# Kernel optimization log

Hardware: AMD Instinct MI355X
Metric: run time of the kernel (lower is better)

Reference implementation:

```python
import math
import jax, jax.numpy as jnp
import numpy as np

B, T, D, H = 4, 2048, 256, 4
DK = D // H
P = 2 * T - 1  # relative position length


def setup_inputs() -> dict:
    key = jax.random.key(0)
    ks = jax.random.split(key, 16)
    s = 0.02
    inp = {
        "query": jax.random.normal(ks[0], (B, T, D), jnp.float32),
        "key": jax.random.normal(ks[1], (B, T, D), jnp.float32),
        "value": jax.random.normal(ks[2], (B, T, D), jnp.float32),
        "pos_emb": jax.random.normal(ks[3], (1, P, D), jnp.float32),
        "mask": jnp.ones((B, 1, T), jnp.int32),
        "Wq": jax.random.normal(ks[4], (D, D), jnp.float32) * s,
        "bq": jnp.zeros((D,), jnp.float32),
        "Wk": jax.random.normal(ks[5], (D, D), jnp.float32) * s,
        "bk": jnp.zeros((D,), jnp.float32),
        "Wv": jax.random.normal(ks[6], (D, D), jnp.float32) * s,
        "bv": jnp.zeros((D,), jnp.float32),
        "Wpos": jax.random.normal(ks[7], (D, D), jnp.float32) * s,
        "pos_bias_u": jax.random.normal(ks[8], (H, DK), jnp.float32) * s,
        "pos_bias_v": jax.random.normal(ks[9], (H, DK), jnp.float32) * s,
        "Wo": jax.random.normal(ks[10], (D, D), jnp.float32) * s,
        "bo": jnp.zeros((D,), jnp.float32),
    }
    return inp


def rel_shift(x):
    # x: (B, H, T, P) with P = 2T-1  ->  (B, H, T, T)
    b, h, t, p = x.shape
    x_pad = jnp.pad(x, ((0, 0), (0, 0), (0, 0), (1, 0)))  # (B,H,T,P+1)
    x_pad = x_pad.reshape(b, h, p + 1, t)
    x = x_pad[:, :, 1:].reshape(b, h, t, p)
    return x[..., : p // 2 + 1]


def reference(query, key, value, pos_emb, mask, Wq, bq, Wk, bk, Wv, bv,
              Wpos, pos_bias_u, pos_bias_v, Wo, bo):
    b = query.shape[0]
    q = (query @ Wq.T + bq).reshape(b, -1, H, DK)              # (B,T,H,DK)
    k = (key @ Wk.T + bk).reshape(b, -1, H, DK).transpose(0, 2, 1, 3)    # (B,H,T,DK)
    v = (value @ Wv.T + bv).reshape(b, -1, H, DK).transpose(0, 2, 1, 3)  # (B,H,T,DK)
    p = (pos_emb @ Wpos.T).reshape(pos_emb.shape[0], -1, H, DK).transpose(0, 2, 1, 3)  # (1,H,P,DK)

    q_u = (q + pos_bias_u).transpose(0, 2, 1, 3)  # (B,H,T,DK)
    q_v = (q + pos_bias_v).transpose(0, 2, 1, 3)

    matrix_ac = jnp.matmul(q_u, k.transpose(0, 1, 3, 2))  # (B,H,T,T)
    matrix_bd = jnp.matmul(q_v, p.transpose(0, 1, 3, 2))  # (B,H,T,P), batch broadcast
    matrix_bd = rel_shift(matrix_bd)                       # (B,H,T,T)

    scores = (matrix_ac + matrix_bd) / math.sqrt(DK)
    m = (mask[:, None] == 0)  # (B,1,1,T) bool
    scores = jnp.where(m, jnp.float32(-1e9), scores)
    attn = jax.nn.softmax(scores, axis=-1)
    attn = jnp.where(m, jnp.float32(0.0), attn)

    x = jnp.matmul(attn, v)                               # (B,H,T,DK)
    x = x.transpose(0, 2, 1, 3).reshape(b, -1, H * DK)    # (B,T,D)
    return x @ Wo.T + bo
```

## Files before the change

### kernel.cpp

```cpp
#include <hip/hip_runtime.h>
#include <hip/hip_bf16.h>
#include <string.h>

#define Bc 4
#define Tc 2048
#define Dc 256
#define Hc 4
#define DKc 64
#define Pc 4095

typedef short bf16x8 __attribute__((ext_vector_type(8)));
typedef float f32x4 __attribute__((ext_vector_type(4)));

__device__ __forceinline__ unsigned short f2bs(float x) {
    __bf16 b = (__bf16)x;
    return __builtin_bit_cast(unsigned short, b);
}
__device__ __forceinline__ float bs2f(unsigned short u) {
    unsigned int x = ((unsigned int)u) << 16;
    return __builtin_bit_cast(float, x);
}

__global__ __launch_bounds__(256) void wsplit_kernel(
    const float* __restrict__ W,
    unsigned short* __restrict__ Whi,
    unsigned short* __restrict__ Wlo)
{
    int i = blockIdx.x * 256 + threadIdx.x;
    if (i >= Dc * Dc) return;
    float w = W[i];
    unsigned short h = f2bs(w);
    Whi[i] = h;
    Wlo[i] = f2bs(w - bs2f(h));
}

__global__ __launch_bounds__(256) void gemm_mfma_proj(
    const float* __restrict__ A,
    const float* __restrict__ Wt,
    const float* __restrict__ bias,
    const float* __restrict__ addv,
    unsigned short* __restrict__ outp,
    int M, int Tdim)
{
    __shared__ unsigned short sa[64 * 72];
    __shared__ unsigned short sb[64 * 72];
    const int tid = threadIdx.x;
    const int wv = tid >> 6, lane = tid & 63;
    const int c = lane & 15, g = lane >> 4;
    const int m0 = blockIdx.x * 64, n0 = blockIdx.y * 64;
    const int tb = wv * 16;

    f32x4 acc[4];
    #pragma unroll
    for (int ct = 0; ct < 4; ct++) acc[ct] = (f32x4){0.f, 0.f, 0.f, 0.f};

    for (int k0 = 0; k0 < 256; k0 += 64) {
        if (k0) __syncthreads();
        #pragma unroll
        for (int r = 0; r < 2; r++) {
            int lin = tid + 256 * r;
            int row = lin >> 3, ch = lin & 7;
            int gm = m0 + row;
            float4 f0, f1;
            if (gm < M) {
                f0 = *(const float4*)(A + (size_t)gm * 256 + k0 + ch * 8);
                f1 = *(const float4*)(A + (size_t)gm * 256 + k0 + ch * 8 + 4);
            } else {
                f0 = make_float4(0.f, 0.f, 0.f, 0.f); f1 = f0;
            }
            unsigned short pa[8] = {f2bs(f0.x), f2bs(f0.y), f2bs(f0.z), f2bs(f0.w),
                                    f2bs(f1.x), f2bs(f1.y), f2bs(f1.z), f2bs(f1.w)};
            *(uint4*)&sa[row * 72 + ch * 8] = *(const uint4*)pa;

            float4 w0 = *(const float4*)(Wt + (size_t)(n0 + row) * 256 + k0 + ch * 8);
            float4 w1 = *(const float4*)(Wt + (size_t)(n0 + row) * 256 + k0 + ch * 8 + 4);
            unsigned short pb[8] = {f2bs(w0.x), f2bs(w0.y), f2bs(w0.z), f2bs(w0.w),
                                    f2bs(w1.x), f2bs(w1.y), f2bs(w1.z), f2bs(w1.w)};
            *(uint4*)&sb[row * 72 + ch * 8] = *(const uint4*)pb;
        }
        __syncthreads();
        #pragma unroll
        for (int kk = 0; kk < 2; kk++) {
            bf16x8 af = *(const bf16x8*)&sa[(tb + c) * 72 + kk * 32 + g * 8];
            #pragma unroll
            for (int ct = 0; ct < 4; ct++) {
                bf16x8 bf = *(const bf16x8*)&sb[(ct * 16 + c) * 72 + kk * 32 + g * 8];
                acc[ct] = __builtin_amdgcn_mfma_f32_16x16x32_bf16(af, bf, acc[ct], 0, 0, 0);
            }
        }
    }

    __syncthreads();
    #pragma unroll
    for (int ct = 0; ct < 4; ct++) {
        int n = n0 + ct * 16 + c;
        float badd = (bias ? bias[n] : 0.f) + (addv ? addv[n] : 0.f);
        #pragma unroll
        for (int r = 0; r < 4; r++)
            sa[(tb + g * 4 + r) * 72 + ct * 16 + c] = f2bs(acc[ct][r] + badd);
    }
    __syncthreads();
    const int hh = n0 >> 6;
    #pragma unroll
    for (int r = 0; r < 2; r++) {
        int lin = tid + 256 * r;
        int row = lin >> 3, ch = lin & 7;
        int gm = m0 + row;
        if (gm >= M) continue;
        int bb = gm / Tdim, t = gm - bb * Tdim;
        size_t oidx = ((size_t)(bb * Hc + hh) * Tdim + t) * DKc + ch * 8;
        *(uint4*)&outp[oidx] = *(const uint4*)&sa[row * 72 + ch * 8];
    }
}

__global__ __launch_bounds__(256) void gemm_out_split(
    const unsigned short* __restrict__ Ahi,
    const unsigned short* __restrict__ Alo,
    const unsigned short* __restrict__ Whi,
    const unsigned short* __restrict__ Wlo,
    const float* __restrict__ bias,
    float* __restrict__ outp, int M)
{
    __shared__ unsigned short sah[64 * 72];
    __shared__ unsigned short sal[64 * 72];
    __shared__ unsigned short sbh[64 * 72];
    __shared__ unsigned short sbl[64 * 72];
    __shared__ float sout[64 * 68];
    const int tid = threadIdx.x;
    const int wv = tid >> 6, lane = tid & 63;
    const int c = lane & 15, g = lane >> 4;
    const int m0 = blockIdx.x * 64, n0 = blockIdx.y * 64;
    const int tb = wv * 16;

    f32x4 acc[4];
    #pragma unroll
    for (int ct = 0; ct < 4; ct++) acc[ct] = (f32x4){0.f, 0.f, 0.f, 0.f};

    for (int k0 = 0; k0 < 256; k0 += 64) {
        if (k0) __syncthreads();
        #pragma unroll
        for (int r = 0; r < 2; r++) {
            int lin = tid + 256 * r;
            int row = lin >> 3, ch = lin & 7;
            size_t asrc = (size_t)(m0 + row) * 256 + k0 + ch * 8;
            size_t wsrc = (size_t)(n0 + row) * 256 + k0 + ch * 8;
            *(uint4*)&sah[row * 72 + ch * 8] = *(const uint4*)(Ahi + asrc);
            *(uint4*)&sal[row * 72 + ch * 8] = *(const uint4*)(Alo + asrc);
            *(uint4*)&sbh[row * 72 + ch * 8] = *(const uint4*)(Whi + wsrc);
            *(uint4*)&sbl[row * 72 + ch * 8] = *(const uint4*)(Wlo + wsrc);
        }
        __syncthreads();
        #pragma unroll
        for (int kk = 0; kk < 2; kk++) {
            bf16x8 ah = *(const bf16x8*)&sah[(tb + c) * 72 + kk * 32 + g * 8];
            bf16x8 al = *(const bf16x8*)&sal[(tb + c) * 72 + kk * 32 + g * 8];
            #pragma unroll
            for (int ct = 0; ct < 4; ct++) {
                bf16x8 bh = *(const bf16x8*)&sbh[(ct * 16 + c) * 72 + kk * 32 + g * 8];
                bf16x8 bl = *(const bf16x8*)&sbl[(ct * 16 + c) * 72 + kk * 32 + g * 8];
                acc[ct] = __builtin_amdgcn_mfma_f32_16x16x32_bf16(ah, bh, acc[ct], 0, 0, 0);
                acc[ct] = __builtin_amdgcn_mfma_f32_16x16x32_bf16(ah, bl, acc[ct], 0, 0, 0);
                acc[ct] = __builtin_amdgcn_mfma_f32_16x16x32_bf16(al, bh, acc[ct], 0, 0, 0);
            }
        }
    }

    __syncthreads();
    #pragma unroll
    for (int ct = 0; ct < 4; ct++) {
        float b = bias[n0 + ct * 16 + c];
        #pragma unroll
        for (int r = 0; r < 4; r++)
            sout[(tb + g * 4 + r) * 68 + ct * 16 + c] = acc[ct][r] + b;
    }
    __syncthreads();
    #pragma unroll
    for (int r = 0; r < 4; r++) {
        int lin = tid + 256 * r;
        int row = lin >> 4, c4 = lin & 15;
        float4 v = *(const float4*)&sout[row * 68 + c4 * 4];
        *(float4*)&outp[(size_t)(m0 + row) * 256 + n0 + c4 * 4] = v;
    }
}

__global__ __launch_bounds__(256) void dpw_kernel(
    const unsigned short* __restrict__ ph,
    const float* __restrict__ pbu,
    const float* __restrict__ pbv,
    float* __restrict__ dpw)
{
    int idx = blockIdx.x * 256 + threadIdx.x;
    if (idx >= Hc * Pc) return;
    int h = idx / Pc;
    const unsigned short* row = ph + (size_t)idx * DKc;
    const float* u = pbu + h * DKc;
    const float* v = pbv + h * DKc;
    float acc = 0.f;
    #pragma unroll
    for (int d = 0; d < DKc; d++)
        acc = fmaf(v[d] - u[d], bs2f(row[d]), acc);
    dpw[idx] = acc;
}

__global__ __launch_bounds__(256) void attn_mfma(
    const unsigned short* __restrict__ qu,
    const unsigned short* __restrict__ kh,
    const unsigned short* __restrict__ vh,
    const unsigned short* __restrict__ ph,
    const float* __restrict__ dpw_g,
    const int*   __restrict__ mask,
    unsigned short* __restrict__ xhi,
    unsigned short* __restrict__ xlo)
{
    __shared__ unsigned short sq[64 * 72];
    __shared__ unsigned short sk[64 * 72];
    __shared__ unsigned short svt[64 * 72];
    __shared__ unsigned short sp[64 * 72];
    __shared__ unsigned short spw[128 * 72];
    __shared__ float sbdw[4][16 * 84];
    __shared__ float sdpw[128];
    __shared__ float smask[64];

    const int tid = threadIdx.x;
    const int wv = tid >> 6;
    const int lane = tid & 63;
    const int c = lane & 15, g = lane >> 4;
    const int bh = blockIdx.x, b = bh >> 2, h = bh & 3;
    const int t0 = blockIdx.y * 64;
    const int tb = wv * 16;

    const unsigned short* qbase = qu + ((size_t)bh * Tc + t0) * DKc;
    const unsigned short* kbase = kh + (size_t)bh * Tc * DKc;
    const unsigned short* vbase = vh + (size_t)bh * Tc * DKc;
    const unsigned short* pbase = ph + (size_t)h * Pc * DKc;

    #pragma unroll
    for (int r = 0; r < 2; r++) {
        int lin = tid + 256 * r;
        int row = lin >> 3, ch = lin & 7;
        *(uint4*)&sq[row * 72 + ch * 8] =
            *(const uint4*)(qbase + (size_t)row * DKc + ch * 8);
    }

    f32x4 O[4];
    #pragma unroll
    for (int ct = 0; ct < 4; ct++) O[ct] = (f32x4){0.f, 0.f, 0.f, 0.f};
    float mrow[4], lrow[4];
    #pragma unroll
    for (int r = 0; r < 4; r++) { mrow[r] = -3.0e38f; lrow[r] = 0.f; }

    bf16x8 qf0, qf1;

    for (int kt = 0; kt < Tc / 64; kt++) {
        const int j0 = kt * 64;
        __syncthreads();

        #pragma unroll
        for (int r = 0; r < 2; r++) {
            int lin = tid + 256 * r;
            int row = lin >> 3, ch = lin & 7;
            *(uint4*)&sk[row * 72 + ch * 8] =
                *(const uint4*)(kbase + (size_t)(j0 + row) * DKc + ch * 8);
        }
        #pragma unroll
        for (int r = 0; r < 2; r++) {
            int lin = tid + 256 * r;
            int trow = lin >> 3, ch = lin & 7;
            uint4 raw = *(const uint4*)(vbase + (size_t)(j0 + trow) * DKc + ch * 8);
            unsigned short el[8];
            __builtin_memcpy(el, &raw, 16);
            #pragma unroll
            for (int e = 0; e < 8; e++) {
                int dk = ch * 8 + e;
                svt[dk * 72 + (trow ^ ((dk >> 3) << 3))] = el[e];
            }
        }
        const int relbase = j0 - t0 + (Tc - 64);
        #pragma unroll
        for (int r = 0; r < 4; r++) {
            int lin = tid + 256 * r;
            int row = lin >> 3, ch = lin & 7;
            int grow = relbase + row;
            if (grow > Pc - 1) grow = Pc - 1;
            *(uint4*)&spw[row * 72 + ch * 8] =
                *(const uint4*)(pbase + (size_t)grow * DKc + ch * 8);
        }
        if (tid < 128) {
            int idx = relbase + tid;
            sdpw[tid] = (idx <= Pc - 1) ? dpw_g[h * Pc + idx] : 0.f;
        }
        if (tid < 64) smask[tid] = (mask[b * Tc + j0 + tid] == 0) ? -1e9f : 0.f;
        __syncthreads();

        if (kt == 0) {
            qf0 = *(const bf16x8*)&sq[(tb + c) * 72 + g * 8];
            qf1 = *(const bf16x8*)&sq[(tb + c) * 72 + (4 + g) * 8];
        }

        f32x4 sac[4];
        #pragma unroll
        for (int ct = 0; ct < 4; ct++) {
            f32x4 acc = (f32x4){0.f, 0.f, 0.f, 0.f};
            bf16x8 kf0 = *(const bf16x8*)&sk[(ct * 16 + c) * 72 + g * 8];
            bf16x8 kf1 = *(const bf16x8*)&sk[(ct * 16 + c) * 72 + (4 + g) * 8];
            acc = __builtin_amdgcn_mfma_f32_16x16x32_bf16(qf0, kf0, acc, 0, 0, 0);
            acc = __builtin_amdgcn_mfma_f32_16x16x32_bf16(qf1, kf1, acc, 0, 0, 0);
            sac[ct] = acc;
        }

        #pragma unroll
        for (int wt = 0; wt < 5; wt++) {
            f32x4 acc = (f32x4){0.f, 0.f, 0.f, 0.f};
            int prow = (48 - tb) + wt * 16 + c;
            bf16x8 pf0 = *(const bf16x8*)&spw[prow * 72 + g * 8];
            bf16x8 pf1 = *(const bf16x8*)&spw[prow * 72 + (4 + g) * 8];
            acc = __builtin_amdgcn_mfma_f32_16x16x32_bf16(qf0, pf0, acc, 0, 0, 0);
            acc = __builtin_amdgcn_mfma_f32_16x16x32_bf16(qf1, pf1, acc, 0, 0, 0);
            float dpwv = sdpw[(48 - tb) + wt * 16 + c];
            #pragma unroll
            for (int r = 0; r < 4; r++)
                sbdw[wv][(g * 4 + r) * 84 + wt * 16 + c] = acc[r] + dpwv;
        }

        float sreg[4][4];
        #pragma unroll
        for (int ct = 0; ct < 4; ct++) {
            float madd = smask[ct * 16 + c];
            #pragma unroll
            for (int r = 0; r < 4; r++) {
                int tt = g * 4 + r;
                int x = ct * 16 + c - tt + 15;
                sreg[ct][r] = (sac[ct][r] + sbdw[wv][tt * 84 + x]) * 0.125f + madd;
            }
        }

        float tmax[4], tsum[4];
        #pragma unroll
        for (int r = 0; r < 4; r++)
            tmax[r] = fmaxf(fmaxf(sreg[0][r], sreg[1][r]), fmaxf(sreg[2][r], sreg[3][r]));
        #pragma unroll
        for (int off = 1; off < 16; off <<= 1)
            #pragma unroll
            for (int r = 0; r < 4; r++)
                tmax[r] = fmaxf(tmax[r], __shfl_xor(tmax[r], off));

        float mnew[4], scl[4];
        #pragma unroll
        for (int r = 0; r < 4; r++) {
            mnew[r] = fmaxf(mrow[r], tmax[r]);
            scl[r] = __expf(mrow[r] - mnew[r]);
        }
        float pr[4][4];
        #pragma unroll
        for (int r = 0; r < 4; r++) {
            #pragma unroll
            for (int ct = 0; ct < 4; ct++)
                pr[ct][r] = __expf(sreg[ct][r] - mnew[r]);
            tsum[r] = (pr[0][r] + pr[1][r]) + (pr[2][r] + pr[3][r]);
        }
        #pragma unroll
        for (int off = 1; off < 16; off <<= 1)
            #pragma unroll
            for (int r = 0; r < 4; r++)
                tsum[r] += __shfl_xor(tsum[r], off);
        #pragma unroll
        for (int r = 0; r < 4; r++) {
            lrow[r] = lrow[r] * scl[r] + tsum[r];
            mrow[r] = mnew[r];
        }
        #pragma unroll
        for (int ct = 0; ct < 4; ct++) {
            f32x4 o = O[ct];
            o[0] *= scl[0]; o[1] *= scl[1]; o[2] *= scl[2]; o[3] *= scl[3];
            O[ct] = o;
        }

        #pragma unroll
        for (int ct = 0; ct < 4; ct++)
            #pragma unroll
            for (int r = 0; r < 4; r++)
                sp[(tb + g * 4 + r) * 72 + ct * 16 + c] = f2bs(pr[ct][r]);

        #pragma unroll
        for (int js = 0; js < 2; js++) {
            bf16x8 pfrag = *(const bf16x8*)&sp[(tb + c) * 72 + (js * 4 + g) * 8];
            #pragma unroll
            for (int ct = 0; ct < 4; ct++) {
                int dk = ct * 16 + c;
                int tcol = (js * 32 + g * 8) ^ ((dk >> 3) << 3);
                bf16x8 vf = *(const bf16x8*)&svt[dk * 72 + tcol];
                O[ct] = __builtin_amdgcn_mfma_f32_16x16x32_bf16(pfrag, vf, O[ct], 0, 0, 0);
            }
        }
    }

    float invl[4];
    #pragma unroll
    for (int r = 0; r < 4; r++)
        invl[r] = (lrow[r] > 0.f) ? 1.f / lrow[r] : 0.f;
    #pragma unroll
    for (int ct = 0; ct < 4; ct++)
        #pragma unroll
        for (int r = 0; r < 4; r++) {
            size_t idx = ((size_t)(b * Tc + t0 + tb + g * 4 + r)) * Dc + h * DKc + ct * 16 + c;
            float v = O[ct][r] * invl[r];
            unsigned short hi = f2bs(v);
            xhi[idx] = hi;
            xlo[idx] = f2bs(v - bs2f(hi));
        }
}

extern "C" void kernel_launch(void* const* d_in, const int* in_sizes, int n_in,
                              void* d_out, int out_size, void* d_ws, size_t ws_size,
                              hipStream_t stream) {
    const float* query   = (const float*)d_in[0];
    const float* key_    = (const float*)d_in[1];
    const float* value   = (const float*)d_in[2];
    const float* pos_emb = (const float*)d_in[3];
    const int*   mask    = (const int*)d_in[4];
    const float* Wq  = (const float*)d_in[5];
    const float* bq  = (const float*)d_in[6];
    const float* Wk  = (const float*)d_in[7];
    const float* bk  = (const float*)d_in[8];
    const float* Wv  = (const float*)d_in[9];
    const float* bv  = (const float*)d_in[10];
    const float* Wpos = (const float*)d_in[11];
    const float* pbu = (const float*)d_in[12];
    const float* pbv = (const float*)d_in[13];
    const float* Wo  = (const float*)d_in[14];
    const float* bo  = (const float*)d_in[15];
    float* out = (float*)d_out;

    const size_t NQ = (size_t)Bc * Hc * Tc * DKc;
    unsigned short* qu_b = (unsigned short*)d_ws;
    unsigned short* kh_b = qu_b + NQ;
    unsigned short* vh_b = kh_b + NQ;
    unsigned short* ph_b = vh_b + NQ;
    unsigned short* xhi  = ph_b + 1048576;
    unsigned short* xlo  = xhi + NQ;
    unsigned short* wo_hi = xlo + NQ;
    unsigned short* wo_lo = wo_hi + 65536;
    float* dpw = (float*)(wo_lo + 65536);

    dim3 blk(256);
    wsplit_kernel<<<dim3(Dc * Dc / 256), blk, 0, stream>>>(Wo, wo_hi, wo_lo);
    gemm_mfma_proj<<<dim3(128, 4), blk, 0, stream>>>(query, Wq, bq, pbu, qu_b, Bc * Tc, Tc);
    gemm_mfma_proj<<<dim3(128, 4), blk, 0, stream>>>(key_,  Wk, bk, nullptr, kh_b, Bc * Tc, Tc);
    gemm_mfma_proj<<<dim3(128, 4), blk, 0, stream>>>(value, Wv, bv, nullptr, vh_b, Bc * Tc, Tc);
    gemm_mfma_proj<<<dim3(64, 4),  blk, 0, stream>>>(pos_emb, Wpos, nullptr, nullptr, ph_b, Pc, Pc);
    dpw_kernel<<<dim3((Hc * Pc + 255) / 256), blk, 0, stream>>>(ph_b, pbu, pbv, dpw);
    attn_mfma<<<dim3(Bc * Hc, Tc / 64), blk, 0, stream>>>(qu_b, kh_b, vh_b, ph_b, dpw, mask, xhi, xlo);
    gemm_out_split<<<dim3(128, 4), blk, 0, stream>>>(xhi, xlo, wo_hi, wo_lo, bo, out, Bc * Tc);
}
```

Measured before the change: 246.9 us.

## Merge launches, fold scale into Q, and register-prefetch K/V/P in attention

Merges the Q/K/V projections into one launch over blockIdx.z and fuses the dpw reduction into the positional projection. The Wo hi/lo split now happens inside the output GEMM, and the 1/sqrt(dk) scale is folded into Q and dpw. The attention loop now prefetches the next K, V and P tiles, plus dpw and mask, into registers while the current tile is computed, and keeps P in a 128-row ring buffer so each step loads 64 new rows instead of 128. The aim is fewer launches and less exposed global-load latency, at the cost of more register pressure and redundant Wo splitting in every output block.

```diff
diff --git a/kernel.cpp b/kernel.cpp
--- a/kernel.cpp
+++ b/kernel.cpp
@@ -21,29 +21,12 @@
     return __builtin_bit_cast(float, x);
 }
 
-__global__ __launch_bounds__(256) void wsplit_kernel(
-    const float* __restrict__ W,
-    unsigned short* __restrict__ Whi,
-    unsigned short* __restrict__ Wlo)
+__device__ __forceinline__ void gemm_body(
+    const float* __restrict__ A, const float* __restrict__ Wt,
+    const float* __restrict__ bias, const float* __restrict__ addv,
+    unsigned short* __restrict__ outp, int M, int Tdim, float scale,
+    unsigned short* sa, unsigned short* sb)
 {
-    int i = blockIdx.x * 256 + threadIdx.x;
-    if (i >= Dc * Dc) return;
-    float w = W[i];
-    unsigned short h = f2bs(w);
-    Whi[i] = h;
-    Wlo[i] = f2bs(w - bs2f(h));
-}
-
-__global__ __launch_bounds__(256) void gemm_mfma_proj(
-    const float* __restrict__ A,
-    const float* __restrict__ Wt,
-    const float* __restrict__ bias,
-    const float* __restrict__ addv,
-    unsigned short* __restrict__ outp,
-    int M, int Tdim)
-{
-    __shared__ unsigned short sa[64 * 72];
-    __shared__ unsigned short sb[64 * 72];
     const int tid = threadIdx.x;
     const int wv = tid >> 6, lane = tid & 63;
     const int c = lane & 15, g = lane >> 4;
@@ -97,7 +80,7 @@
         float badd = (bias ? bias[n] : 0.f) + (addv ? addv[n] : 0.f);
         #pragma unroll
         for (int r = 0; r < 4; r++)
-            sa[(tb + g * 4 + r) * 72 + ct * 16 + c] = f2bs(acc[ct][r] + badd);
+            sa[(tb + g * 4 + r) * 72 + ct * 16 + c] = f2bs((acc[ct][r] + badd) * scale);
     }
     __syncthreads();
     const int hh = n0 >> 6;
@@ -113,11 +96,51 @@
     }
 }
 
+__global__ __launch_bounds__(256) void gemm_qkv(
+    const float* __restrict__ q, const float* __restrict__ k, const float* __restrict__ v,
+    const float* __restrict__ Wq, const float* __restrict__ bq,
+    const float* __restrict__ Wk, const float* __restrict__ bk,
+    const float* __restrict__ Wv, const float* __restrict__ bv,
+    const float* __restrict__ pbu,
+    unsigned short* __restrict__ qo, unsigned short* __restrict__ ko,
+    unsigned short* __restrict__ vo)
+{
+    __shared__ unsigned short sa[64 * 72];
+    __shared__ unsigned short sb[64 * 72];
+    const float *A, *Wt, *bias, *addv; unsigned short* outp; float scale;
+    if (blockIdx.z == 0)      { A = q; Wt = Wq; bias = bq; addv = pbu;    outp = qo; scale = 0.125f; }
+    else if (blockIdx.z == 1) { A = k; Wt = Wk; bias = bk; addv = nullptr; outp = ko; scale = 1.f; }
+    else                      { A = v; Wt = Wv; bias = bv; addv = nullptr; outp = vo; scale = 1.f; }
+    gemm_body(A, Wt, bias, addv, outp, Bc * Tc, Tc, scale, sa, sb);
+}
+
+__global__ __launch_bounds__(256) void gemm_p(
+    const float* __restrict__ pos_emb, const float* __restrict__ Wpos,
+    const float* __restrict__ pbu, const float* __restrict__ pbv,
+    unsigned short* __restrict__ ph_b, float* __restrict__ dpw)
+{
+    __shared__ unsigned short sa[64 * 72];
+    __shared__ unsigned short sb[64 * 72];
+    gemm_body(pos_emb, Wpos, nullptr, nullptr, ph_b, Pc, Pc, 1.f, sa, sb);
+    const int tid = threadIdx.x;
+    const int m0 = blockIdx.x * 64, h = blockIdx.y;
+    if (tid < 64) {
+        int w = m0 + tid;
+        if (w < Pc) {
+            float acc = 0.f;
+            #pragma unroll
+            for (int dk = 0; dk < DKc; dk++)
+                acc = fmaf(pbv[h * DKc + dk] - pbu[h * DKc + dk],
+                           bs2f(sa[tid * 72 + dk]), acc);
+            dpw[h * Pc + w] = acc * 0.125f;
+        }
+    }
+}
+
 __global__ __launch_bounds__(256) void gemm_out_split(
     const unsigned short* __restrict__ Ahi,
     const unsigned short* __restrict__ Alo,
-    const unsigned short* __restrict__ Whi,
-    const unsigned short* __restrict__ Wlo,
+    const float* __restrict__ Wo,
     const float* __restrict__ bias,
     float* __restrict__ outp, int M)
 {
@@ -143,11 +166,20 @@
             int lin = tid + 256 * r;
             int row = lin >> 3, ch = lin & 7;
             size_t asrc = (size_t)(m0 + row) * 256 + k0 + ch * 8;
-            size_t wsrc = (size_t)(n0 + row) * 256 + k0 + ch * 8;
             *(uint4*)&sah[row * 72 + ch * 8] = *(const uint4*)(Ahi + asrc);
             *(uint4*)&sal[row * 72 + ch * 8] = *(const uint4*)(Alo + asrc);
-            *(uint4*)&sbh[row * 72 + ch * 8] = *(const uint4*)(Whi + wsrc);
-            *(uint4*)&sbl[row * 72 + ch * 8] = *(const uint4*)(Wlo + wsrc);
+            float4 w0 = *(const float4*)(Wo + (size_t)(n0 + row) * 256 + k0 + ch * 8);
+            float4 w1 = *(const float4*)(Wo + (size_t)(n0 + row) * 256 + k0 + ch * 8 + 4);
+            float we[8] = {w0.x, w0.y, w0.z, w0.w, w1.x, w1.y, w1.z, w1.w};
+            unsigned short phi[8], plo[8];
+            #pragma unroll
+            for (int e = 0; e < 8; e++) {
+                unsigned short hi = f2bs(we[e]);
+                phi[e] = hi;
+                plo[e] = f2bs(we[e] - bs2f(hi));
+            }
+            *(uint4*)&sbh[row * 72 + ch * 8] = *(const uint4*)phi;
+            *(uint4*)&sbl[row * 72 + ch * 8] = *(const uint4*)plo;
         }
         __syncthreads();
         #pragma unroll
@@ -181,25 +213,6 @@
         float4 v = *(const float4*)&sout[row * 68 + c4 * 4];
         *(float4*)&outp[(size_t)(m0 + row) * 256 + n0 + c4 * 4] = v;
     }
-}
-
-__global__ __launch_bounds__(256) void dpw_kernel(
-    const unsigned short* __restrict__ ph,
-    const float* __restrict__ pbu,
-    const float* __restrict__ pbv,
-    float* __restrict__ dpw)
-{
-    int idx = blockIdx.x * 256 + threadIdx.x;
-    if (idx >= Hc * Pc) return;
-    int h = idx / Pc;
-    const unsigned short* row = ph + (size_t)idx * DKc;
-    const float* u = pbu + h * DKc;
-    const float* v = pbv + h * DKc;
-    float acc = 0.f;
-    #pragma unroll
-    for (int d = 0; d < DKc; d++)
-        acc = fmaf(v[d] - u[d], bs2f(row[d]), acc);
-    dpw[idx] = acc;
 }
 
 __global__ __launch_bounds__(256) void attn_mfma(
@@ -228,18 +241,38 @@
     const int bh = blockIdx.x, b = bh >> 2, h = bh & 3;
     const int t0 = blockIdx.y * 64;
     const int tb = wv * 16;
+    const int base0 = Tc - 64 - t0;
 
     const unsigned short* qbase = qu + ((size_t)bh * Tc + t0) * DKc;
     const unsigned short* kbase = kh + (size_t)bh * Tc * DKc;
     const unsigned short* vbase = vh + (size_t)bh * Tc * DKc;
     const unsigned short* pbase = ph + (size_t)h * Pc * DKc;
 
+    const int srow = tid >> 3, sch = tid & 7;
+
     #pragma unroll
     for (int r = 0; r < 2; r++) {
-        int lin = tid + 256 * r;
-        int row = lin >> 3, ch = lin & 7;
-        *(uint4*)&sq[row * 72 + ch * 8] =
-            *(const uint4*)(qbase + (size_t)row * DKc + ch * 8);
+        int row = srow + r * 32;
+        *(uint4*)&sq[row * 72 + sch * 8] =
+            *(const uint4*)(qbase + (size_t)row * DKc + sch * 8);
+        int a0 = base0 + row;
+        *(uint4*)&spw[(a0 & 127) * 72 + sch * 8] =
+            *(const uint4*)(pbase + (size_t)a0 * DKc + sch * 8);
+    }
+    if (tid < 64) sdpw[(base0 + tid) & 127] = dpw_g[h * Pc + base0 + tid];
+
+    uint4 kreg[2], vreg[2], preg[2];
+    float dpwreg = 0.f; int mreg = 1;
+    #pragma unroll
+    for (int r = 0; r < 2; r++) {
+        int row = srow + r * 32;
+        kreg[r] = *(const uint4*)(kbase + (size_t)row * DKc + sch * 8);
+        vreg[r] = *(const uint4*)(vbase + (size_t)row * DKc + sch * 8);
+        preg[r] = *(const uint4*)(pbase + (size_t)(base0 + 64 + row) * DKc + sch * 8);
+    }
+    if (tid < 64) {
+        dpwreg = dpw_g[h * Pc + base0 + 64 + tid];
+        mreg = mask[b * Tc + tid];
     }
 
     f32x4 O[4];
@@ -252,45 +285,43 @@
     bf16x8 qf0, qf1;
 
     for (int kt = 0; kt < Tc / 64; kt++) {
-        const int j0 = kt * 64;
+        const int relb = base0 + kt * 64;
         __syncthreads();
 
         #pragma unroll
         for (int r = 0; r < 2; r++) {
-            int lin = tid + 256 * r;
-            int row = lin >> 3, ch = lin & 7;
-            *(uint4*)&sk[row * 72 + ch * 8] =
-                *(const uint4*)(kbase + (size_t)(j0 + row) * DKc + ch * 8);
-        }
-        #pragma unroll
-        for (int r = 0; r < 2; r++) {
-            int lin = tid + 256 * r;
-            int trow = lin >> 3, ch = lin & 7;
-            uint4 raw = *(const uint4*)(vbase + (size_t)(j0 + trow) * DKc + ch * 8);
+            int row = srow + r * 32;
+            *(uint4*)&sk[row * 72 + sch * 8] = kreg[r];
             unsigned short el[8];
-            __builtin_memcpy(el, &raw, 16);
+            __builtin_memcpy(el, &vreg[r], 16);
             #pragma unroll
             for (int e = 0; e < 8; e++) {
-                int dk = ch * 8 + e;
-                svt[dk * 72 + (trow ^ ((dk >> 3) << 3))] = el[e];
-            }
-        }
-        const int relbase = j0 - t0 + (Tc - 64);
-        #pragma unroll
-        for (int r = 0; r < 4; r++) {
-            int lin = tid + 256 * r;
-            int row = lin >> 3, ch = lin & 7;
-            int grow = relbase + row;
-            if (grow > Pc - 1) grow = Pc - 1;
-            *(uint4*)&spw[row * 72 + ch * 8] =
-                *(const uint4*)(pbase + (size_t)grow * DKc + ch * 8);
-        }
-        if (tid < 128) {
-            int idx = relbase + tid;
-            sdpw[tid] = (idx <= Pc - 1) ? dpw_g[h * Pc + idx] : 0.f;
-        }
-        if (tid < 64) smask[tid] = (mask[b * Tc + j0 + tid] == 0) ? -1e9f : 0.f;
+                int dk = sch * 8 + e;
+                svt[dk * 72 + (row ^ ((dk >> 3) << 3))] = el[e];
+            }
+            *(uint4*)&spw[((relb + 64 + row) & 127) * 72 + sch * 8] = preg[r];
+        }
+        if (tid < 64) {
+            sdpw[(relb + 64 + tid) & 127] = dpwreg;
+            smask[tid] = (mreg == 0) ? -1e9f : 0.f;
+        }
         __syncthreads();
+
+        if (kt < Tc / 64 - 1) {
+            const int j0n = (kt + 1) * 64;
+            const int relbn = relb + 64;
+            #pragma unroll
+            for (int r = 0; r < 2; r++) {
+                int row = srow + r * 32;
+                kreg[r] = *(const uint4*)(kbase + (size_t)(j0n + row) * DKc + sch * 8);
+                vreg[r] = *(const uint4*)(vbase + (size_t)(j0n + row) * DKc + sch * 8);
+                preg[r] = *(const uint4*)(pbase + (size_t)(relbn + 64 + row) * DKc + sch * 8);
+            }
+            if (tid < 64) {
+                dpwreg = dpw_g[h * Pc + relbn + 64 + tid];
+                mreg = mask[b * Tc + j0n + tid];
+            }
+        }
 
         if (kt == 0) {
             qf0 = *(const bf16x8*)&sq[(tb + c) * 72 + g * 8];
@@ -311,12 +342,13 @@
         #pragma unroll
         for (int wt = 0; wt < 5; wt++) {
             f32x4 acc = (f32x4){0.f, 0.f, 0.f, 0.f};
-            int prow = (48 - tb) + wt * 16 + c;
-            bf16x8 pf0 = *(const bf16x8*)&spw[prow * 72 + g * 8];
-            bf16x8 pf1 = *(const bf16x8*)&spw[prow * 72 + (4 + g) * 8];
+            int wlog = (48 - tb) + wt * 16 + c;
+            int phys = (relb + wlog) & 127;
+            bf16x8 pf0 = *(const bf16x8*)&spw[phys * 72 + g * 8];
+            bf16x8 pf1 = *(const bf16x8*)&spw[phys * 72 + (4 + g) * 8];
             acc = __builtin_amdgcn_mfma_f32_16x16x32_bf16(qf0, pf0, acc, 0, 0, 0);
             acc = __builtin_amdgcn_mfma_f32_16x16x32_bf16(qf1, pf1, acc, 0, 0, 0);
-            float dpwv = sdpw[(48 - tb) + wt * 16 + c];
+            float dpwv = sdpw[phys];
             #pragma unroll
             for (int r = 0; r < 4; r++)
                 sbdw[wv][(g * 4 + r) * 84 + wt * 16 + c] = acc[r] + dpwv;
@@ -330,7 +362,7 @@
             for (int r = 0; r < 4; r++) {
                 int tt = g * 4 + r;
                 int x = ct * 16 + c - tt + 15;
-                sreg[ct][r] = (sac[ct][r] + sbdw[wv][tt * 84 + x]) * 0.125f + madd;
+                sreg[ct][r] = sac[ct][r] + sbdw[wv][tt * 84 + x] + madd;
             }
         }
 
@@ -438,17 +470,12 @@
     unsigned short* ph_b = vh_b + NQ;
     unsigned short* xhi  = ph_b + 1048576;
     unsigned short* xlo  = xhi + NQ;
-    unsigned short* wo_hi = xlo + NQ;
-    unsigned short* wo_lo = wo_hi + 65536;
-    float* dpw = (float*)(wo_lo + 65536);
+    float* dpw = (float*)(xlo + NQ);
 
     dim3 blk(256);
-    wsplit_kernel<<<dim3(Dc * Dc / 256), blk, 0, stream>>>(Wo, wo_hi, wo_lo);
-    gemm_mfma_proj<<<dim3(128, 4), blk, 0, stream>>>(query, Wq, bq, pbu, qu_b, Bc * Tc, Tc);
-    gemm_mfma_proj<<<dim3(128, 4), blk, 0, stream>>>(key_,  Wk, bk, nullptr, kh_b, Bc * Tc, Tc);
-    gemm_mfma_proj<<<dim3(128, 4), blk, 0, stream>>>(value, Wv, bv, nullptr, vh_b, Bc * Tc, Tc);
-    gemm_mfma_proj<<<dim3(64, 4),  blk, 0, stream>>>(pos_emb, Wpos, nullptr, nullptr, ph_b, Pc, Pc);
-    dpw_kernel<<<dim3((Hc * Pc + 255) / 256), blk, 0, stream>>>(ph_b, pbu, pbv, dpw);
+    gemm_qkv<<<dim3(128, 4, 3), blk, 0, stream>>>(query, key_, value,
+        Wq, bq, Wk, bk, Wv, bv, pbu, qu_b, kh_b, vh_b);
+    gemm_p<<<dim3(64, 4), blk, 0, stream>>>(pos_emb, Wpos, pbu, pbv, ph_b, dpw);
     attn_mfma<<<dim3(Bc * Hc, Tc / 64), blk, 0, stream>>>(qu_b, kh_b, vh_b, ph_b, dpw, mask, xhi, xlo);
-    gemm_out_split<<<dim3(128, 4), blk, 0, stream>>>(xhi, xlo, wo_hi, wo_lo, bo, out, Bc * Tc);
-}
+    gemm_out_split<<<dim3(128, 4), blk, 0, stream>>>(xhi, xlo, Wo, bo, out, Bc * Tc);
+}
```

Result: no change. 245.8 us (-0.4%).
